# Optimization experiments

Hardware: AMD Instinct MI355X
Metric: run time of the kernel (lower is better)

## Reference

```python
import jax, jax.numpy as jnp
import numpy as np

NUM_HEADS = 8
ATTN_DIM = 512
DIM_HEAD = ATTN_DIM // NUM_HEADS
SCALE = DIM_HEAD ** -0.5
GN_EPS = 1e-5


def setup_inputs() -> dict:
    key = jax.random.key(0)
    k1, k2, k3 = jax.random.split(key, 3)
    B, H, W, C_IN, C_OUT = 8, 32, 32, 256, 256
    x = jax.random.normal(k1, (B, H, W, C_IN), dtype=jnp.float32)
    w_qkv = jax.random.normal(k2, (C_IN, 3 * ATTN_DIM), dtype=jnp.float32) * (C_IN ** -0.5)
    w_out = jax.random.normal(k3, (ATTN_DIM, C_OUT), dtype=jnp.float32) * (ATTN_DIM ** -0.5)
    b_out = jnp.zeros((C_OUT,), dtype=jnp.float32)
    gamma = jnp.ones((C_OUT,), dtype=jnp.float32)
    beta = jnp.zeros((C_OUT,), dtype=jnp.float32)
    return {"x": x, "w_qkv": w_qkv, "w_out": w_out, "b_out": b_out, "gamma": gamma, "beta": beta}


def reference(x, w_qkv, w_out, b_out, gamma, beta):
    B, H, W, _ = x.shape
    N = H * W
    # 1x1 conv QKV projection (no bias)
    qkv = jnp.einsum('bhwc,cd->bhwd', x, w_qkv)
    q, k, v = jnp.split(qkv, 3, axis=-1)
    # NHWC -> (B, heads, dim_head, HW), matching tf transpose+reshape
    def to_heads(t):
        return t.transpose(0, 3, 1, 2).reshape(B, NUM_HEADS, DIM_HEAD, N)
    q = to_heads(q) * SCALE
    k = to_heads(k)
    v = to_heads(v)
    # sim = q^T k over dim_head: (B, heads, N_q, N_k)
    sim = jnp.einsum('bhcn,bhcm->bhnm', q, k)
    attn = jax.nn.softmax(sim, axis=-1)  # includes the max-subtraction of the original
    # out = attn @ v^T: (B, heads, N, dim_head)
    out = jnp.einsum('bhnm,bhcm->bhnc', attn, v)
    # faithful tf.reshape((B,-1,H,W)) then NCHW->NHWC transpose
    out = out.reshape(B, -1, H, W).transpose(0, 2, 3, 1)  # (B, H, W, attn_dim)
    # output 1x1 conv (with bias) + GroupNorm(groups=1): normalize over (H, W, C) per sample
    y = jnp.einsum('bhwc,cd->bhwd', out, w_out) + b_out
    mean = jnp.mean(y, axis=(1, 2, 3), keepdims=True)
    var = jnp.var(y, axis=(1, 2, 3), keepdims=True)
    y = (y - mean) * jax.lax.rsqrt(var + GN_EPS)
    return y * gamma + beta
```

## Files before the change

kernel.cpp:

```cpp
#include <hip/hip_runtime.h>
#include <math.h>

#define NPOS   1024
#define CIN    256
#define DQKV   1536
#define ATTND  512
#define HEADS  8
#define DH     64
#define COUT   256
#define NBATCH 8
#define SCALE  0.125f
#define GN_EPS 1e-5f

typedef __attribute__((ext_vector_type(8))) __bf16 bf16x8;
typedef __attribute__((ext_vector_type(4))) __bf16 bf16x4;
typedef __attribute__((ext_vector_type(4))) float floatx4;
typedef __attribute__((ext_vector_type(8))) unsigned short ushort8;

#if __has_builtin(__builtin_amdgcn_exp2f)
#define EXP2(x) __builtin_amdgcn_exp2f(x)
#else
#define EXP2(x) exp2f(x)
#endif

#define GLOAD16(G, L) __builtin_amdgcn_global_load_lds( \
    (const __attribute__((address_space(1))) void*)(G), \
    (__attribute__((address_space(3))) void*)(L), 16, 0, 0)

#define OFF_XB   (0ull)
#define OFF_WT   (4ull*1048576)
#define OFF_WOT  (4ull*1048576 + 786432ull)
#define OFF_QB   (5ull*1048576)
#define OFF_KB   (13ull*1048576)
#define OFF_VT   (29ull*1048576)
#define OFF_O2TT (45ull*1048576)
#define OFF_ST   (53ull*1048576)

__device__ inline ushort8 cvt_bf8(float4 a, float4 b) {
    bf16x8 o;
    o[0] = (__bf16)a.x; o[1] = (__bf16)a.y; o[2] = (__bf16)a.z; o[3] = (__bf16)a.w;
    o[4] = (__bf16)b.x; o[5] = (__bf16)b.y; o[6] = (__bf16)b.z; o[7] = (__bf16)b.w;
    return *(ushort8*)&o;
}

__global__ __launch_bounds__(256) void prep(
    const float* __restrict__ x,
    const float* __restrict__ w_qkv, const float* __restrict__ w_out,
    unsigned short* __restrict__ xb,
    unsigned short* __restrict__ wT, unsigned short* __restrict__ woT,
    float* __restrict__ stats)
{
    const int bid = blockIdx.x;
    const int t = threadIdx.x;
    __shared__ unsigned short tile[64][68];

    if (bid == 0) stats[t] = 0.0f;

    if (bid >= 128) {
        const size_t base = (size_t)(bid - 128) * 8192 + (size_t)t * 8;
        #pragma unroll
        for (int i = 0; i < 4; ++i) {
            const size_t off = base + (size_t)i * 2048;
            const float4 u = *(const float4*)&x[off];
            const float4 v = *(const float4*)&x[off + 4];
            *(ushort8*)&xb[off] = cvt_bf8(u, v);
        }
        return;
    }

    if (bid < 96) {
        const int n0 = (bid >> 2) * 64, k0 = (bid & 3) * 64;
        #pragma unroll
        for (int p = 0; p < 4; ++p) {
            const int row = p * 16 + (t >> 4);
            const int c = (t & 15) * 4;
            float4 a = *(const float4*)&w_qkv[(size_t)(k0 + row) * DQKV + n0 + c];
            float sv[4] = {a.x, a.y, a.z, a.w};
            #pragma unroll
            for (int j = 0; j < 4; ++j) {
                const float sc = (n0 + c + j) < 512 ? (SCALE * 1.44269504088896f) : 1.0f;
                __bf16 hb = (__bf16)(sv[j] * sc);
                tile[row][c + j] = *(unsigned short*)&hb;
            }
        }
        __syncthreads();
        const int nn = t >> 2;
        const int kc = (t & 3) * 16;
        unsigned short tmp[16];
        #pragma unroll
        for (int j = 0; j < 16; ++j) tmp[j] = tile[kc + j][nn];
        *(ushort8*)&wT[(size_t)(n0 + nn) * 256 + k0 + kc]     = *(ushort8*)&tmp[0];
        *(ushort8*)&wT[(size_t)(n0 + nn) * 256 + k0 + kc + 8] = *(ushort8*)&tmp[8];
        return;
    }

    const int idx = bid - 96;
    const int d0 = (idx & 3) * 64, k0 = (idx >> 2) * 64;
    #pragma unroll
    for (int p = 0; p < 4; ++p) {
        const int row = p * 16 + (t >> 4);
        const int c = (t & 15) * 4;
        float4 a = *(const float4*)&w_out[(size_t)(k0 + row) * COUT + d0 + c];
        float sv[4] = {a.x, a.y, a.z, a.w};
        #pragma unroll
        for (int j = 0; j < 4; ++j) {
            __bf16 hb = (__bf16)sv[j];
            tile[row][c + j] = *(unsigned short*)&hb;
        }
    }
    __syncthreads();
    {
        const int nn = t >> 2;
        const int kc = (t & 3) * 16;
        unsigned short tmp[16];
        #pragma unroll
        for (int j = 0; j < 16; ++j) tmp[j] = tile[kc + j][nn];
        *(ushort8*)&woT[(size_t)(d0 + nn) * 512 + k0 + kc]     = *(ushort8*)&tmp[0];
        *(ushort8*)&woT[(size_t)(d0 + nn) * 512 + k0 + kc + 8] = *(ushort8*)&tmp[8];
    }
}

__global__ __launch_bounds__(256) void qkv_gemm_mfma(
    const unsigned short* __restrict__ xb, const __bf16* __restrict__ wT,
    __bf16* __restrict__ qb, __bf16* __restrict__ kb, __bf16* __restrict__ vT)
{
    const int bid = blockIdx.x;
    const int xcd = bid & 7, local = bid >> 3;
    const int m0 = (xcd * 8 + (local & 7)) * 128;
    const int n0 = (local >> 3) * 128;

    const int t = threadIdx.x;
    const int w = t >> 6, lane = t & 63;
    const int col = lane & 15, qd = lane >> 4;
    const int wm = w >> 1, wn = w & 1;

    __shared__ __align__(16) unsigned short As[128][40];
    __shared__ __align__(16) unsigned short Bs[128][40];

    floatx4 zero4 = {0.f, 0.f, 0.f, 0.f};
    floatx4 acc[4][4];
    #pragma unroll
    for (int i = 0; i < 4; ++i)
        #pragma unroll
        for (int j = 0; j < 4; ++j) acc[i][j] = zero4;

    const int lrow = t >> 2, lc8 = (t & 3) * 8;

    ushort8 areg[2], breg[2];
    areg[0] = *(const ushort8*)&xb[(size_t)(m0 + lrow) * 256 + lc8];
    areg[1] = *(const ushort8*)&xb[(size_t)(m0 + lrow + 64) * 256 + lc8];
    breg[0] = *(const ushort8*)&wT[(size_t)(n0 + lrow) * 256 + lc8];
    breg[1] = *(const ushort8*)&wT[(size_t)(n0 + lrow + 64) * 256 + lc8];

    for (int kk = 0; kk < 8; ++kk) {
        __syncthreads();
        *(ushort8*)&As[lrow][lc8]      = areg[0];
        *(ushort8*)&As[lrow + 64][lc8] = areg[1];
        *(ushort8*)&Bs[lrow][lc8]      = breg[0];
        *(ushort8*)&Bs[lrow + 64][lc8] = breg[1];
        __syncthreads();
        const int kn = (kk < 7) ? (kk + 1) * 32 : 0;
        areg[0] = *(const ushort8*)&xb[(size_t)(m0 + lrow) * 256 + kn + lc8];
        areg[1] = *(const ushort8*)&xb[(size_t)(m0 + lrow + 64) * 256 + kn + lc8];
        breg[0] = *(const ushort8*)&wT[(size_t)(n0 + lrow) * 256 + kn + lc8];
        breg[1] = *(const ushort8*)&wT[(size_t)(n0 + lrow + 64) * 256 + kn + lc8];

        bf16x8 wf[4];
        #pragma unroll
        for (int ct = 0; ct < 4; ++ct)
            wf[ct] = *(const bf16x8*)&Bs[wn * 64 + ct * 16 + col][qd * 8];
        #pragma unroll
        for (int st = 0; st < 4; ++st) {
            bf16x8 xf = *(const bf16x8*)&As[wm * 64 + st * 16 + col][qd * 8];
            #pragma unroll
            for (int ct = 0; ct < 4; ++ct)
                acc[ct][st] = __builtin_amdgcn_mfma_f32_16x16x32_bf16(wf[ct], xf, acc[ct][st], 0, 0, 0);
        }
    }

    #pragma unroll
    for (int ct = 0; ct < 4; ++ct) {
        const int cbase = n0 + wn * 64 + ct * 16;
        const int sect = cbase >> 9;
        const int hh = (cbase >> 6) & 7;
        const int dd = (cbase & 63) + qd * 4;
        if (sect < 2) {
            __bf16* base = (sect == 0) ? qb : kb;
            #pragma unroll
            for (int st = 0; st < 4; ++st) {
                const int m = m0 + wm * 64 + st * 16 + col;
                const int b_ = m >> 10, n = m & 1023;
                bf16x4 o;
                #pragma unroll
                for (int r = 0; r < 4; ++r) o[r] = (__bf16)acc[ct][st][r];
                *(bf16x4*)&base[(((size_t)b_ * HEADS + hh) * NPOS + n) * DH + dd] = o;
            }
        } else {
            #pragma unroll
            for (int st = 0; st < 4; ++st) {
                const int m = m0 + wm * 64 + st * 16 + col;
                const int b_ = m >> 10, n = m & 1023;
                const size_t rowbase = ((size_t)(b_ * HEADS + hh) * DH + dd) * NPOS + n;
                #pragma unroll
                for (int r = 0; r < 4; ++r)
                    vT[rowbase + (size_t)r * NPOS] = (__bf16)acc[ct][st][r];
            }
        }
    }
}

__global__ __launch_bounds__(256, 2) void attn_mfma(
    const __bf16* __restrict__ qg, const __bf16* __restrict__ kg,
    const __bf16* __restrict__ vTg, __bf16* __restrict__ o2tT)
{
    const int bid = blockIdx.x;
    const int rid = (bid & 7) * 64 + (bid >> 3);
    const int qblk = rid & 7, h = (rid >> 3) & 7, b = rid >> 6;
    const int bh = b * HEADS + h;
    const int t = threadIdx.x;
    const int w = t >> 6, lane = t & 63;
    const int col = lane & 15;
    const int qd = lane >> 4;

    __shared__ __align__(16) unsigned short Kbuf[2][64][64];
    __shared__ __align__(16) unsigned short Vbuf[2][64][64];
    __shared__ __align__(16) unsigned short ps[4][32][68];

    bf16x8 qf0[2], qf1[2];
    #pragma unroll
    for (int s = 0; s < 2; ++s) {
        const __bf16* qptr = qg + ((size_t)bh * NPOS + qblk * 128 + s * 64 + w * 16 + col) * DH;
        qf0[s] = *(const bf16x8*)(qptr + qd * 8);
        qf1[s] = *(const bf16x8*)(qptr + 32 + qd * 8);
    }

    const char* kByte = (const char*)kg  + (size_t)bh * NPOS * DH * 2;
    const char* vByte = (const char*)vTg + (size_t)bh * DH * NPOS * 2;
    const int rsub = lane >> 3;
    const int csw  = ((lane & 7) * 16) ^ (rsub << 4);
    const char* ksrc0 = kByte + (size_t)(w * 8 + rsub) * 128  + csw;
    const char* vsrc0 = vByte + (size_t)(w * 8 + rsub) * 2048 + csw;

#define STAGE(B, KT) do {                                                    \
    const char* ks_ = ksrc0 + (size_t)(KT) * 8192;                           \
    const char* vs_ = vsrc0 + (size_t)(KT) * 128;                            \
    GLOAD16(ks_,         &Kbuf[B][0][0] + w * 512);                          \
    GLOAD16(ks_ + 4096,  &Kbuf[B][0][0] + 2048 + w * 512);                   \
    GLOAD16(vs_,         &Vbuf[B][0][0] + w * 512);                          \
    GLOAD16(vs_ + 65536, &Vbuf[B][0][0] + 2048 + w * 512);                   \
} while (0)

    floatx4 zero4 = {0.f, 0.f, 0.f, 0.f};
    floatx4 accO[2][4];
    #pragma unroll
    for (int s = 0; s < 2; ++s)
        #pragma unroll
        for (int i = 0; i < 4; ++i) accO[s][i] = zero4;
    floatx4 accL[2] = {zero4, zero4};
    bf16x8 ones8;
    #pragma unroll
    for (int j = 0; j < 8; ++j) ones8[j] = (__bf16)1.0f;

    const int swzc = (col & 7) << 4;
    const int offF0 = (qd * 16) ^ swzc;
    const int offF1 = (64 + qd * 16) ^ swzc;

    STAGE(0, 0);
    __syncthreads();

    int cur = 0;
    for (int kt = 0; kt < 16; ++kt) {
        if (kt < 15) STAGE(cur ^ 1, kt + 1);

        floatx4 accS[2][4];
        #pragma unroll
        for (int mt = 0; mt < 4; ++mt) {
            const char* krow = (const char*)&Kbuf[cur][mt * 16 + col][0];
            bf16x8 kf0 = *(const bf16x8*)(krow + offF0);
            bf16x8 kf1 = *(const bf16x8*)(krow + offF1);
            #pragma unroll
            for (int s = 0; s < 2; ++s) {
                accS[s][mt] = __builtin_amdgcn_mfma_f32_16x16x32_bf16(kf0, qf0[s], zero4, 0, 0, 0);
                accS[s][mt] = __builtin_amdgcn_mfma_f32_16x16x32_bf16(kf1, qf1[s], accS[s][mt], 0, 0, 0);
            }
        }

        #pragma unroll
        for (int s = 0; s < 2; ++s)
            #pragma unroll
            for (int mt = 0; mt < 4; ++mt) {
                bf16x4 pv;
                #pragma unroll
                for (int r = 0; r < 4; ++r) pv[r] = (__bf16)EXP2(accS[s][mt][r]);
                *(bf16x4*)&ps[w][s * 16 + col][mt * 16 + qd * 4] = pv;
            }

        bf16x8 pf0[2], pf1[2];
        #pragma unroll
        for (int s = 0; s < 2; ++s) {
            pf0[s] = *(const bf16x8*)&ps[w][s * 16 + col][qd * 8];
            pf1[s] = *(const bf16x8*)&ps[w][s * 16 + col][32 + qd * 8];
            accL[s] = __builtin_amdgcn_mfma_f32_16x16x32_bf16(ones8, pf0[s], accL[s], 0, 0, 0);
            accL[s] = __builtin_amdgcn_mfma_f32_16x16x32_bf16(ones8, pf1[s], accL[s], 0, 0, 0);
        }

        #pragma unroll
        for (int ct = 0; ct < 4; ++ct) {
            const char* vrow = (const char*)&Vbuf[cur][ct * 16 + col][0];
            bf16x8 vf0 = *(const bf16x8*)(vrow + offF0);
            bf16x8 vf1 = *(const bf16x8*)(vrow + offF1);
            #pragma unroll
            for (int s = 0; s < 2; ++s) {
                accO[s][ct] = __builtin_amdgcn_mfma_f32_16x16x32_bf16(vf0, pf0[s], accO[s][ct], 0, 0, 0);
                accO[s][ct] = __builtin_amdgcn_mfma_f32_16x16x32_bf16(vf1, pf1[s], accO[s][ct], 0, 0, 0);
            }
        }
        __syncthreads();
        cur ^= 1;
    }
#undef STAGE

    float inv_l[2];
    #pragma unroll
    for (int s = 0; s < 2; ++s) inv_l[s] = 1.0f / accL[s][0];

    unsigned short (*obuf)[8][68] = (unsigned short (*)[8][68])ps;
    __syncthreads();
    #pragma unroll
    for (int s = 0; s < 2; ++s)
        #pragma unroll
        for (int ct = 0; ct < 4; ++ct) {
            bf16x4 o;
            #pragma unroll
            for (int r = 0; r < 4; ++r) o[r] = (__bf16)(accO[s][ct][r] * inv_l[s]);
            *(bf16x4*)&obuf[col][s * 4 + w][ct * 16 + qd * 4] = o;
        }
    __syncthreads();
    const int chbase = h * 64 + qblk * 8;
    #pragma unroll
    for (int i = 0; i < 4; ++i) {
        const int p = i * 256 + t;
        const int pc = p >> 6, cc = p & 63;
        bf16x8 o;
        #pragma unroll
        for (int j = 0; j < 8; ++j) {
            unsigned short u = obuf[pc][j][cc];
            o[j] = *(__bf16*)&u;
        }
        *(bf16x8*)&o2tT[((size_t)b * NPOS + p) * ATTND + chbase] = o;
    }
}

__global__ __launch_bounds__(256) void out_mfma(
    const __bf16* __restrict__ a, const __bf16* __restrict__ woT,
    const float* __restrict__ b_out, float* __restrict__ y,
    float* __restrict__ stats)
{
    const int t = threadIdx.x;
    const int w = t >> 6, lane = t & 63;
    const int col = lane & 15, qd = lane >> 4;
    const int wm = w >> 1, wn = w & 1;
    const int m0 = blockIdx.x * 64, d0 = blockIdx.y * 64;
    const int b = blockIdx.x >> 4;

    __shared__ __align__(16) unsigned short As[64][72];
    __shared__ __align__(16) unsigned short Bs[64][72];
    __shared__ float reds[4], redq[4];

    floatx4 zero4 = {0.f, 0.f, 0.f, 0.f};
    floatx4 acc[2][2];
    #pragma unroll
    for (int i = 0; i < 2; ++i)
        #pragma unroll
        for (int j = 0; j < 2; ++j) acc[i][j] = zero4;

    const int lrow = t >> 2, lc = (t & 3) * 16;

    for (int k0 = 0; k0 < ATTND; k0 += 64) {
        __syncthreads();
        *(ushort8*)&As[lrow][lc]     = *(const ushort8*)&a[(size_t)(m0 + lrow) * ATTND + k0 + lc];
        *(ushort8*)&As[lrow][lc + 8] = *(const ushort8*)&a[(size_t)(m0 + lrow) * ATTND + k0 + lc + 8];
        *(ushort8*)&Bs[lrow][lc]     = *(const ushort8*)&woT[(size_t)(d0 + lrow) * ATTND + k0 + lc];
        *(ushort8*)&Bs[lrow][lc + 8] = *(const ushort8*)&woT[(size_t)(d0 + lrow) * ATTND + k0 + lc + 8];
        __syncthreads();
        bf16x8 af0[2], af1[2];
        #pragma unroll
        for (int mt = 0; mt < 2; ++mt) {
            af0[mt] = *(const bf16x8*)&As[wm * 32 + mt * 16 + col][qd * 8];
            af1[mt] = *(const bf16x8*)&As[wm * 32 + mt * 16 + col][32 + qd * 8];
        }
        #pragma unroll
        for (int nt = 0; nt < 2; ++nt) {
            bf16x8 bf0 = *(const bf16x8*)&Bs[wn * 32 + nt * 16 + col][qd * 8];
            bf16x8 bf1 = *(const bf16x8*)&Bs[wn * 32 + nt * 16 + col][32 + qd * 8];
            #pragma unroll
            for (int mt = 0; mt < 2; ++mt) {
                acc[mt][nt] = __builtin_amdgcn_mfma_f32_16x16x32_bf16(af0[mt], bf0, acc[mt][nt], 0, 0, 0);
                acc[mt][nt] = __builtin_amdgcn_mfma_f32_16x16x32_bf16(af1[mt], bf1, acc[mt][nt], 0, 0, 0);
            }
        }
    }

    float bias_n[2];
    #pragma unroll
    for (int nt = 0; nt < 2; ++nt) bias_n[nt] = b_out[d0 + wn * 32 + nt * 16 + col];

    float bsum = 0.0f, bsq = 0.0f;
    #pragma unroll
    for (int mt = 0; mt < 2; ++mt) {
        #pragma unroll
        for (int r = 0; r < 4; ++r) {
            const int m = m0 + wm * 32 + mt * 16 + qd * 4 + r;
            const int p = m & 1023;
            #pragma unroll
            for (int nt = 0; nt < 2; ++nt) {
                const int d = d0 + wn * 32 + nt * 16 + col;
                const float v = acc[mt][nt][r] + bias_n[nt];
                y[((size_t)b * NPOS + p) * COUT + d] = v;
                bsum += v;
                bsq  += v * v;
            }
        }
    }
    #pragma unroll
    for (int off = 1; off < 64; off <<= 1) {
        bsum += __shfl_xor(bsum, off);
        bsq  += __shfl_xor(bsq, off);
    }
    if (lane == 0) { reds[w] = bsum; redq[w] = bsq; }
    __syncthreads();
    if (t == 0) {
        atomicAdd(&stats[b * 16],       reds[0] + reds[1] + reds[2] + reds[3]);
        atomicAdd(&stats[128 + b * 16], redq[0] + redq[1] + redq[2] + redq[3]);
    }
}

__global__ __launch_bounds__(256) void gn_finalize(
    float* __restrict__ y, const float* __restrict__ stats,
    const float* __restrict__ gamma, const float* __restrict__ beta)
{
    const int idx = blockIdx.x * 256 + threadIdx.x;
    const int e = idx * 4;
    const int b_ = e >> 18;
    const int d = e & (COUT - 1);
    const float invn = 1.0f / (float)(NPOS * COUT);
    const float mean = stats[b_ * 16] * invn;
    const float var  = stats[128 + b_ * 16] * invn - mean * mean;
    const float rsig = rsqrtf(var + GN_EPS);
    float4 vv = *(float4*)&y[e];
    const float4 g  = *(const float4*)&gamma[d];
    const float4 bt = *(const float4*)&beta[d];
    vv.x = (vv.x - mean) * rsig * g.x + bt.x;
    vv.y = (vv.y - mean) * rsig * g.y + bt.y;
    vv.z = (vv.z - mean) * rsig * g.z + bt.z;
    vv.w = (vv.w - mean) * rsig * g.w + bt.w;
    *(float4*)&y[e] = vv;
}

extern "C" void kernel_launch(void* const* d_in, const int* in_sizes, int n_in,
                              void* d_out, int out_size, void* d_ws, size_t ws_size,
                              hipStream_t stream)
{
    const float* x     = (const float*)d_in[0];
    const float* w_qkv = (const float*)d_in[1];
    const float* w_out = (const float*)d_in[2];
    const float* b_out = (const float*)d_in[3];
    const float* gamma = (const float*)d_in[4];
    const float* beta  = (const float*)d_in[5];
    float* out = (float*)d_out;
    char* ws = (char*)d_ws;

    unsigned short* xb  = (unsigned short*)(ws + OFF_XB);
    unsigned short* wT  = (unsigned short*)(ws + OFF_WT);
    unsigned short* woT = (unsigned short*)(ws + OFF_WOT);
    __bf16* qb  = (__bf16*)(ws + OFF_QB);
    __bf16* kb  = (__bf16*)(ws + OFF_KB);
    __bf16* vT  = (__bf16*)(ws + OFF_VT);
    __bf16* o2tT = (__bf16*)(ws + OFF_O2TT);
    float* stats = (float*)(ws + OFF_ST);

    prep         <<<dim3(384),     256, 0, stream>>>(x, w_qkv, w_out, xb, wT, woT, stats);
    qkv_gemm_mfma<<<dim3(768),     256, 0, stream>>>(xb, (const __bf16*)wT, qb, kb, vT);
    attn_mfma    <<<dim3(512),     256, 0, stream>>>(qb, kb, vT, o2tT);
    out_mfma     <<<dim3(128, 4),  256, 0, stream>>>(o2tT, (const __bf16*)woT, b_out, out, stats);
    gn_finalize  <<<dim3(2048),    256, 0, stream>>>(out, stats, gamma, beta);
}
```

Baseline: 125.8 us.

## Double-buffer QKV GEMM with direct global-to-LDS loads and XCD-aware out_mfma mapping

New measurement: 124.6 us. No clear change (-1.0%).

```diff
diff --git a/kernel.cpp b/kernel.cpp
--- a/kernel.cpp
+++ b/kernel.cpp
@@ -134,8 +134,8 @@
     const int col = lane & 15, qd = lane >> 4;
     const int wm = w >> 1, wn = w & 1;
 
-    __shared__ __align__(16) unsigned short As[128][40];
-    __shared__ __align__(16) unsigned short Bs[128][40];
+    __shared__ __align__(16) unsigned short As[2][128][32];
+    __shared__ __align__(16) unsigned short Bs[2][128][32];
 
     floatx4 zero4 = {0.f, 0.f, 0.f, 0.f};
     floatx4 acc[4][4];
@@ -144,39 +144,43 @@
         #pragma unroll
         for (int j = 0; j < 4; ++j) acc[i][j] = zero4;
 
-    const int lrow = t >> 2, lc8 = (t & 3) * 8;
-
-    ushort8 areg[2], breg[2];
-    areg[0] = *(const ushort8*)&xb[(size_t)(m0 + lrow) * 256 + lc8];
-    areg[1] = *(const ushort8*)&xb[(size_t)(m0 + lrow + 64) * 256 + lc8];
-    breg[0] = *(const ushort8*)&wT[(size_t)(n0 + lrow) * 256 + lc8];
-    breg[1] = *(const ushort8*)&wT[(size_t)(n0 + lrow + 64) * 256 + lc8];
-
+    const int arow = lane >> 2;
+    const int soff = (((lane & 3) ^ ((lane >> 3) & 3)) << 4);
+    const char* xsrc = (const char*)xb + (size_t)(m0 + w * 16 + arow) * 512 + soff;
+    const char* wsrc = (const char*)wT + (size_t)(n0 + w * 16 + arow) * 512 + soff;
+
+#define QSTAGE(B, KK) do {                                            \
+    GLOAD16(xsrc + (KK) * 64,             &As[B][w * 16][0]);         \
+    GLOAD16(xsrc + 32768 + (KK) * 64,     &As[B][64 + w * 16][0]);    \
+    GLOAD16(wsrc + (KK) * 64,             &Bs[B][w * 16][0]);         \
+    GLOAD16(wsrc + 32768 + (KK) * 64,     &Bs[B][64 + w * 16][0]);    \
+} while (0)
+
+    QSTAGE(0, 0);
+    __syncthreads();
+
+    const int rsw = ((col >> 1) & 3);
+    const int fro = ((qd ^ rsw) << 4);
+
+    int cur = 0;
     for (int kk = 0; kk < 8; ++kk) {
-        __syncthreads();
-        *(ushort8*)&As[lrow][lc8]      = areg[0];
-        *(ushort8*)&As[lrow + 64][lc8] = areg[1];
-        *(ushort8*)&Bs[lrow][lc8]      = breg[0];
-        *(ushort8*)&Bs[lrow + 64][lc8] = breg[1];
-        __syncthreads();
-        const int kn = (kk < 7) ? (kk + 1) * 32 : 0;
-        areg[0] = *(const ushort8*)&xb[(size_t)(m0 + lrow) * 256 + kn + lc8];
-        areg[1] = *(const ushort8*)&xb[(size_t)(m0 + lrow + 64) * 256 + kn + lc8];
-        breg[0] = *(const ushort8*)&wT[(size_t)(n0 + lrow) * 256 + kn + lc8];
-        breg[1] = *(const ushort8*)&wT[(size_t)(n0 + lrow + 64) * 256 + kn + lc8];
+        if (kk < 7) QSTAGE(cur ^ 1, kk + 1);
 
         bf16x8 wf[4];
         #pragma unroll
         for (int ct = 0; ct < 4; ++ct)
-            wf[ct] = *(const bf16x8*)&Bs[wn * 64 + ct * 16 + col][qd * 8];
+            wf[ct] = *(const bf16x8*)((const char*)&Bs[cur][wn * 64 + ct * 16 + col][0] + fro);
         #pragma unroll
         for (int st = 0; st < 4; ++st) {
-            bf16x8 xf = *(const bf16x8*)&As[wm * 64 + st * 16 + col][qd * 8];
+            bf16x8 xf = *(const bf16x8*)((const char*)&As[cur][wm * 64 + st * 16 + col][0] + fro);
             #pragma unroll
             for (int ct = 0; ct < 4; ++ct)
                 acc[ct][st] = __builtin_amdgcn_mfma_f32_16x16x32_bf16(wf[ct], xf, acc[ct][st], 0, 0, 0);
         }
-    }
+        __syncthreads();
+        cur ^= 1;
+    }
+#undef QSTAGE
 
     #pragma unroll
     for (int ct = 0; ct < 4; ++ct) {
@@ -356,12 +360,16 @@
     const float* __restrict__ b_out, float* __restrict__ y,
     float* __restrict__ stats)
 {
+    const int bid = blockIdx.x;
+    const int xcd = bid & 7, local = bid >> 3;
+    const int m0 = (xcd * 16 + (local & 15)) * 64;
+    const int d0 = (local >> 4) * 64;
+    const int b = xcd;
+
     const int t = threadIdx.x;
     const int w = t >> 6, lane = t & 63;
     const int col = lane & 15, qd = lane >> 4;
     const int wm = w >> 1, wn = w & 1;
-    const int m0 = blockIdx.x * 64, d0 = blockIdx.y * 64;
-    const int b = blockIdx.x >> 4;
 
     __shared__ __align__(16) unsigned short As[64][72];
     __shared__ __align__(16) unsigned short Bs[64][72];
@@ -479,9 +487,9 @@
     __bf16* o2tT = (__bf16*)(ws + OFF_O2TT);
     float* stats = (float*)(ws + OFF_ST);
 
-    prep         <<<dim3(384),     256, 0, stream>>>(x, w_qkv, w_out, xb, wT, woT, stats);
-    qkv_gemm_mfma<<<dim3(768),     256, 0, stream>>>(xb, (const __bf16*)wT, qb, kb, vT);
-    attn_mfma    <<<dim3(512),     256, 0, stream>>>(qb, kb, vT, o2tT);
-    out_mfma     <<<dim3(128, 4),  256, 0, stream>>>(o2tT, (const __bf16*)woT, b_out, out, stats);
-    gn_finalize  <<<dim3(2048),    256, 0, stream>>>(out, stats, gamma, beta);
-}
+    prep         <<<dim3(384),  256, 0, stream>>>(x, w_qkv, w_out, xb, wT, woT, stats);
+    qkv_gemm_mfma<<<dim3(768),  256, 0, stream>>>(xb, (const __bf16*)wT, qb, kb, vT);
+    attn_mfma    <<<dim3(512),  256, 0, stream>>>(qb, kb, vT, o2tT);
+    out_mfma     <<<dim3(512),  256, 0, stream>>>(o2tT, (const __bf16*)woT, b_out, out, stats);
+    gn_finalize  <<<dim3(2048), 256, 0, stream>>>(out, stats, gamma, beta);
+}
```
